# Optimization experiments

Hardware: AMD Instinct MI355X
Metric: run time of the kernel (lower is better)

## Reference

```python
import jax, jax.numpy as jnp
import numpy as np

N, IN_F, OUT_F = 8192, 512, 256
ALPHA = 0.2  # LeakyReLU negative slope
NEG_INF = -9e15


def setup_inputs() -> dict:
    key = jax.random.key(0)
    k1, k2, k3, k4 = jax.random.split(key, 4)
    input = jax.random.normal(k1, (N, IN_F), dtype=jnp.float32)
    adj = jax.random.randint(k2, (N, N), 0, 2, dtype=jnp.int32)
    # Xavier-like scale for params
    W = jax.random.normal(k3, (IN_F, OUT_F), dtype=jnp.float32) * (1.414 * np.sqrt(2.0 / (IN_F + OUT_F)))
    a = jax.random.normal(k4, (2 * OUT_F, 1), dtype=jnp.float32) * (1.414 * np.sqrt(2.0 / (2 * OUT_F + 1)))
    return {"input": input, "adj": adj, "W": W, "a": a}


def reference(input, adj, W, a):
    h = input @ W                                   # [N, F]
    a1, a2 = a[:OUT_F, 0], a[OUT_F:, 0]             # [F], [F]
    # e[i, j] = leakyrelu(h_i . a1 + h_j . a2) -- equivalent to concat+linear
    s1 = h @ a1                                     # [N]
    s2 = h @ a2                                     # [N]
    e = jax.nn.leaky_relu(s1[:, None] + s2[None, :], negative_slope=ALPHA)  # [N, N]
    e = jnp.where(adj > 0, e, NEG_INF)
    attention = jax.nn.softmax(e, axis=1)           # row-wise softmax
    # dropout p=0.0 / eval mode -> identity
    h_prime = attention @ h                          # [N, F]
    return jax.nn.elu(h_prime)                       # concat=True -> elu
```

## Files before the change

### kernel.cpp

```cpp
#include <hip/hip_runtime.h>
#include <stdint.h>

#define N_NODES 8192
#define IN_FEAT 512
#define OUT_FEAT 256
#define LOG2E 1.4426950408889634f

typedef __bf16 b16x8 __attribute__((ext_vector_type(8)));
typedef unsigned short u16x8v __attribute__((ext_vector_type(8)));
typedef float f32x4 __attribute__((ext_vector_type(4)));
typedef float f32x16 __attribute__((ext_vector_type(16)));

static __device__ __forceinline__ unsigned short f2bf(float f) {
    union { float f; uint32_t u; } v; v.f = f;
    uint32_t r = v.u + 0x7FFFu + ((v.u >> 16) & 1u);
    return (unsigned short)(r >> 16);
}
static __device__ __forceinline__ float bf2f(unsigned short s) {
    union { uint32_t u; float f; } v; v.u = ((uint32_t)s) << 16;
    return v.f;
}

__global__ __launch_bounds__(256) void k0_transpose_w(const float* __restrict__ W,
                                                      unsigned short* __restrict__ Wt) {
    int tid = blockIdx.x * 256 + threadIdx.x;
    int c = tid & (OUT_FEAT - 1);
    int k = tid >> 8;
    Wt[(size_t)c * IN_FEAT + k] = f2bf(W[(size_t)k * OUT_FEAT + c]);
}

__global__ __launch_bounds__(256) void k1_hgemm(const float* __restrict__ input,
                                                const unsigned short* __restrict__ Wt,
                                                const float* __restrict__ a_vec,
                                                unsigned short* __restrict__ hTf32,
                                                float* __restrict__ s1_raw,
                                                float* __restrict__ s2_raw) {
    int tid = threadIdx.x;
    int lane = tid & 63;
    int c = lane & 15, g = lane >> 4;
    int r0 = blockIdx.x * 64 + (tid >> 6) * 16;
    f32x4 acc[16];
#pragma unroll
    for (int t = 0; t < 16; ++t) acc[t] = (f32x4){0.f, 0.f, 0.f, 0.f};
    const float* arow = input + (size_t)(r0 + c) * IN_FEAT;
#pragma unroll 1
    for (int kk = 0; kk < IN_FEAT / 32; ++kk) {
        int kb = kk * 32 + 8 * g;
        float4 x0 = *(const float4*)(arow + kb);
        float4 x1 = *(const float4*)(arow + kb + 4);
        u16x8v au;
        au[0] = f2bf(x0.x); au[1] = f2bf(x0.y); au[2] = f2bf(x0.z); au[3] = f2bf(x0.w);
        au[4] = f2bf(x1.x); au[5] = f2bf(x1.y); au[6] = f2bf(x1.z); au[7] = f2bf(x1.w);
        b16x8 af = __builtin_bit_cast(b16x8, au);
#pragma unroll
        for (int t = 0; t < 16; ++t) {
            b16x8 bf = __builtin_bit_cast(b16x8,
                *(const u16x8v*)(Wt + (size_t)(16 * t + c) * IN_FEAT + kb));
            acc[t] = __builtin_amdgcn_mfma_f32_16x16x32_bf16(af, bf, acc[t], 0, 0, 0);
        }
    }
    float a1v[16], a2v[16];
#pragma unroll
    for (int t = 0; t < 16; ++t) {
        a1v[t] = a_vec[16 * t + c];
        a2v[t] = a_vec[OUT_FEAT + 16 * t + c];
    }
#pragma unroll
    for (int r = 0; r < 4; ++r) {
        float s1p = 0.f, s2p = 0.f;
#pragma unroll
        for (int t = 0; t < 16; ++t) { s1p += acc[t][r] * a1v[t]; s2p += acc[t][r] * a2v[t]; }
#pragma unroll
        for (int m = 1; m <= 8; m <<= 1) { s1p += __shfl_xor(s1p, m); s2p += __shfl_xor(s2p, m); }
        if (c == 0) {
            int row = r0 + 4 * g + r;
            s1_raw[row] = s1p;
            s2_raw[row] = s2p;
        }
    }
    int chunk16 = r0 >> 4;
    int lane_base = c + 32 * (g >> 1);
    int e0 = 4 * (g & 1);
#pragma unroll
    for (int t = 0; t < 16; ++t) {
        ushort4 pk;
        pk.x = f2bf(acc[t][0]); pk.y = f2bf(acc[t][1]);
        pk.z = f2bf(acc[t][2]); pk.w = f2bf(acc[t][3]);
        int lane_t = 16 * (t & 1) + lane_base;
        *(ushort4*)(hTf32 + ((size_t)(chunk16 * 8 + (t >> 1)) * 64 + lane_t) * 8 + e0) = pk;
    }
}

__global__ __launch_bounds__(256) void k2_prep(const float* __restrict__ s1_raw,
                                               const float* __restrict__ s2_raw,
                                               float* __restrict__ e12,
                                               float2* __restrict__ row2) {
    __shared__ float red[256];
    int tid = threadIdx.x;
    float m = -3.0e38f;
    for (int j = tid; j < N_NODES; j += 256) m = fmaxf(m, s2_raw[j]);
    red[tid] = m;
    __syncthreads();
    for (int s = 128; s > 0; s >>= 1) {
        if (tid < s) red[tid] = fmaxf(red[tid], red[tid + s]);
        __syncthreads();
    }
    float M2 = red[0];
    int i = blockIdx.x * 256 + tid;
    float s1 = s1_raw[i];
    float u = s1 + M2;
    float mi = fmaxf(u, 0.2f * u);
    row2[i] = make_float2(__builtin_amdgcn_exp2f((s1 - mi) * LOG2E),
                          __builtin_amdgcn_exp2f((0.2f * s1 - mi) * LOG2E));
    float s2 = s2_raw[i];
    e12[2 * i]     = __builtin_amdgcn_exp2f(s2 * LOG2E);
    e12[2 * i + 1] = __builtin_amdgcn_exp2f(0.2f * s2 * LOG2E);
}

__global__ __launch_bounds__(256, 4) void k3_flash(const int* __restrict__ adj,
                                                   const unsigned short* __restrict__ hTf32,
                                                   const float* __restrict__ e12g,
                                                   const float2* __restrict__ row2,
                                                   unsigned short* __restrict__ poutb,
                                                   float* __restrict__ rowpart) {
    __shared__ __align__(16) float le12[2048];
    __shared__ __align__(16) unsigned short laf[8][512];
    __shared__ __align__(16) uint32_t lmask[32 * 36];
    __shared__ float lsum[4][64];

    int tid = threadIdx.x;
    int cq = tid >> 6, lane = tid & 63;
    int lr = lane & 31, lo = lane >> 5;
    int jq = blockIdx.x & 7;
    int rg = blockIdx.x >> 3;
    int rowbase = rg * 32;

    *(float4*)&le12[tid * 8]     = *(const float4*)(e12g + (size_t)jq * 2048 + tid * 8);
    *(float4*)&le12[tid * 8 + 4] = *(const float4*)(e12g + (size_t)jq * 2048 + tid * 8 + 4);

#pragma unroll 4
    for (int it = 0; it < 16; ++it) {
        int b = it * 256 + tid;
        int row = b >> 7;
        int bir = b & 127;
        const int4* src = (const int4*)(adj + (size_t)(rowbase + row) * N_NODES
                                        + jq * 1024 + bir * 8);
        int4 v0 = src[0];
        int4 v1 = src[1];
        unsigned pb = (unsigned)(v0.x != 0) | ((unsigned)(v0.y != 0) << 1)
                    | ((unsigned)(v0.z != 0) << 2) | ((unsigned)(v0.w != 0) << 3)
                    | ((unsigned)(v1.x != 0) << 4) | ((unsigned)(v1.y != 0) << 5)
                    | ((unsigned)(v1.z != 0) << 6) | ((unsigned)(v1.w != 0) << 7);
        ((unsigned char*)lmask)[row * 144 + bir] = (unsigned char)pb;
    }
    float2 rc = row2[rowbase + lr];
    float E1r = rc.x, E2r = rc.y;
    __syncthreads();

    f32x16 acc0 = {0}, acc1 = {0};
    float lacc = 0.f;

#pragma unroll 1
    for (int kc8 = 0; kc8 < 8; ++kc8) {
        int4 mq = *(const int4*)((const char*)lmask + lr * 144 + kc8 * 16);
        uint32_t md[4] = {(uint32_t)mq.x, (uint32_t)mq.y, (uint32_t)mq.z, (uint32_t)mq.w};

#pragma unroll
        for (int hh = 0; hh < 2; ++hh) {
            int sl = hh * 4 + cq;
            int kc = kc8 * 8 + sl;
            float ev[16];
#pragma unroll
            for (int q = 0; q < 4; ++q)
                *(f32x4*)&ev[q * 4] = *(const f32x4*)&le12[(kc * 16 + 8 * lo) * 2 + q * 4];
            uint32_t mb = (md[sl >> 1] >> (16 * (sl & 1) + 8 * lo)) & 0xFFu;
            b16x8 af;
#pragma unroll
            for (int e = 0; e < 8; ++e) {
                float q0 = fmaxf(E1r * ev[2 * e], E2r * ev[2 * e + 1]);
                float p = (mb & (1u << e)) ? q0 : 0.f;
                lacc += p;
                af[e] = (__bf16)p;
            }
            *(u16x8v*)&laf[sl][lane * 8] = __builtin_bit_cast(u16x8v, af);
        }
        __syncthreads();

        int gchunk0 = jq * 64 + kc8 * 8;
#pragma unroll
        for (int s = 0; s < 8; ++s) {
            const unsigned short* tb =
                hTf32 + ((size_t)((gchunk0 + s) * 8 + 2 * cq) * 64 + lane) * 8;
            b16x8 bf0 = __builtin_bit_cast(b16x8, *(const u16x8v*)(tb));
            b16x8 bf1 = __builtin_bit_cast(b16x8, *(const u16x8v*)(tb + 512));
            b16x8 afs = __builtin_bit_cast(b16x8, *(const u16x8v*)&laf[s][lane * 8]);
            acc0 = __builtin_amdgcn_mfma_f32_32x32x16_bf16(afs, bf0, acc0, 0, 0, 0);
            acc1 = __builtin_amdgcn_mfma_f32_32x32x16_bf16(afs, bf1, acc1, 0, 0, 0);
        }
        __syncthreads();
    }

    lsum[cq][lane] = lacc;
    __syncthreads();
    if (cq == 0) {
        float l = lsum[0][lane] + lsum[1][lane] + lsum[2][lane] + lsum[3][lane];
        float ltot = l + __shfl_xor(l, 32);
        if (lo == 0) rowpart[jq * N_NODES + rowbase + lr] = ltot;
    }

#pragma unroll
    for (int reg = 0; reg < 16; ++reg) {
        int row = (reg & 3) + 8 * (reg >> 2) + 4 * lo;
        size_t base = ((size_t)jq * N_NODES + rowbase + row) * OUT_FEAT + cq * 64 + lr;
        poutb[base] = f2bf(acc0[reg]);
        poutb[base + 32] = f2bf(acc1[reg]);
    }
}

__global__ __launch_bounds__(256) void k4_reduce(const unsigned short* __restrict__ poutb,
                                                 const float* __restrict__ rowpart,
                                                 float* __restrict__ out) {
    int t = blockIdx.x * 256 + threadIdx.x;
    int row = t >> 8;
    float s = 0.f, l = 0.f;
#pragma unroll
    for (int q = 0; q < 8; ++q) {
        s += bf2f(poutb[(size_t)q * N_NODES * OUT_FEAT + t]);
        l += rowpart[q * N_NODES + row];
    }
    float inv = (l > 0.f) ? 1.0f / l : 0.f;
    float x = s * inv;
    out[t] = (x > 0.f) ? x : (__builtin_amdgcn_exp2f(x * LOG2E) - 1.0f);
}

extern "C" void kernel_launch(void* const* d_in, const int* in_sizes, int n_in,
                              void* d_out, int out_size, void* d_ws, size_t ws_size,
                              hipStream_t stream) {
    const float* input = (const float*)d_in[0];
    const int* adj = (const int*)d_in[1];
    const float* W = (const float*)d_in[2];
    const float* a_vec = (const float*)d_in[3];
    float* out = (float*)d_out;

    char* ws = (char*)d_ws;
    unsigned short* Wt    = (unsigned short*)(ws);
    unsigned short* hTf32 = (unsigned short*)(ws + 262144);
    float*  e12     = (float*)(ws + 4456448);
    float2* row2    = (float2*)(ws + 4521984);
    float*  s1_raw  = (float*)(ws + 4587520);
    float*  s2_raw  = (float*)(ws + 4620288);
    float*  rowpart = (float*)(ws + 4653056);
    unsigned short* poutb = (unsigned short*)(ws + 4915200);

    hipLaunchKernelGGL(k0_transpose_w, dim3(512), dim3(256), 0, stream, W, Wt);
    hipLaunchKernelGGL(k1_hgemm, dim3(N_NODES / 64), dim3(256), 0, stream,
                       input, Wt, a_vec, hTf32, s1_raw, s2_raw);
    hipLaunchKernelGGL(k2_prep, dim3(32), dim3(256), 0, stream, s1_raw, s2_raw, e12, row2);
    hipLaunchKernelGGL(k3_flash, dim3(2048), dim3(256), 0, stream,
                       adj, hTf32, e12, row2, poutb, rowpart);
    hipLaunchKernelGGL(k4_reduce, dim3(N_NODES * OUT_FEAT / 256), dim3(256), 0, stream,
                       poutb, rowpart, out);
}
```

Measured before the change: 155.0 us.

## Stream adjacency mask per chunk with double-buffered LDS prefetch

The whole 32x1024 adjacency tile is no longer loaded and packed into a bitmask in the prologue. Each thread now prefetches the 128-column slice for the next kc8 iteration into registers, packs it into one of two small LDS mask buffers after the MFMA phase, and the existing end-of-iteration barrier covers the handoff. This aims to overlap the large int32 adjacency reads with the exp/MFMA work and to shrink LDS use. The cost is extra live registers, around 16 ints, which could lower occupancy under the 4-block launch bound.

```diff
diff --git a/kernel.cpp b/kernel.cpp
--- a/kernel.cpp
+++ b/kernel.cpp
@@ -125,7 +125,7 @@
                                                    float* __restrict__ rowpart) {
     __shared__ __align__(16) float le12[2048];
     __shared__ __align__(16) unsigned short laf[8][512];
-    __shared__ __align__(16) uint32_t lmask[32 * 36];
+    __shared__ __align__(16) uint32_t lmask[2][32][4];
     __shared__ float lsum[4][64];
 
     int tid = threadIdx.x;
@@ -135,23 +135,31 @@
     int rg = blockIdx.x >> 3;
     int rowbase = rg * 32;
 
+    int srow = tid >> 3;
+    int sjb = tid & 7;
+    const int* adjbase = adj + (size_t)(rowbase + srow) * N_NODES + jq * 1024 + sjb * 16;
+
     *(float4*)&le12[tid * 8]     = *(const float4*)(e12g + (size_t)jq * 2048 + tid * 8);
     *(float4*)&le12[tid * 8 + 4] = *(const float4*)(e12g + (size_t)jq * 2048 + tid * 8 + 4);
 
-#pragma unroll 4
-    for (int it = 0; it < 16; ++it) {
-        int b = it * 256 + tid;
-        int row = b >> 7;
-        int bir = b & 127;
-        const int4* src = (const int4*)(adj + (size_t)(rowbase + row) * N_NODES
-                                        + jq * 1024 + bir * 8);
-        int4 v0 = src[0];
-        int4 v1 = src[1];
-        unsigned pb = (unsigned)(v0.x != 0) | ((unsigned)(v0.y != 0) << 1)
-                    | ((unsigned)(v0.z != 0) << 2) | ((unsigned)(v0.w != 0) << 3)
-                    | ((unsigned)(v1.x != 0) << 4) | ((unsigned)(v1.y != 0) << 5)
-                    | ((unsigned)(v1.z != 0) << 6) | ((unsigned)(v1.w != 0) << 7);
-        ((unsigned char*)lmask)[row * 144 + bir] = (unsigned char)pb;
+#define PACK16(BUF, V)                                                                   \
+    {                                                                                    \
+        unsigned pb = 0;                                                                 \
+        _Pragma("unroll")                                                                \
+        for (int k = 0; k < 4; ++k) {                                                    \
+            pb |= ((unsigned)((V)[k].x != 0) << (4 * k))                                 \
+                | ((unsigned)((V)[k].y != 0) << (4 * k + 1))                             \
+                | ((unsigned)((V)[k].z != 0) << (4 * k + 2))                             \
+                | ((unsigned)((V)[k].w != 0) << (4 * k + 3));                            \
+        }                                                                                \
+        *(unsigned short*)((char*)&lmask[BUF][srow][0] + sjb * 2) = (unsigned short)pb;  \
+    }
+
+    {
+        int4 v[4];
+#pragma unroll
+        for (int k = 0; k < 4; ++k) v[k] = *(const int4*)(adjbase + 4 * k);
+        PACK16(0, v)
     }
     float2 rc = row2[rowbase + lr];
     float E1r = rc.x, E2r = rc.y;
@@ -162,9 +170,17 @@
 
 #pragma unroll 1
     for (int kc8 = 0; kc8 < 8; ++kc8) {
-        int4 mq = *(const int4*)((const char*)lmask + lr * 144 + kc8 * 16);
+        int cur = kc8 & 1;
+
+        int4 v[4];
+        if (kc8 < 7) {
+#pragma unroll
+            for (int k = 0; k < 4; ++k)
+                v[k] = *(const int4*)(adjbase + (kc8 + 1) * 128 + 4 * k);
+        }
+
+        int4 mq = *(const int4*)&lmask[cur][lr][0];
         uint32_t md[4] = {(uint32_t)mq.x, (uint32_t)mq.y, (uint32_t)mq.z, (uint32_t)mq.w};
-
 #pragma unroll
         for (int hh = 0; hh < 2; ++hh) {
             int sl = hh * 4 + cq;
@@ -197,8 +213,11 @@
             acc0 = __builtin_amdgcn_mfma_f32_32x32x16_bf16(afs, bf0, acc0, 0, 0, 0);
             acc1 = __builtin_amdgcn_mfma_f32_32x32x16_bf16(afs, bf1, acc1, 0, 0, 0);
         }
+
+        if (kc8 < 7) PACK16(cur ^ 1, v)
         __syncthreads();
     }
+#undef PACK16
 
     lsum[cq][lane] = lacc;
     __syncthreads();
```

Result: faster. 150.9 us (-2.7%).
